# Optimization experiments

Measured on AMD Instinct MI355X. Metric: run time of the kernel, lower is better.

## Reference

```python
import jax, jax.numpy as jnp
import numpy as np

PARAMETER = 0.1
INPUT_SIZE = 512
OUTPUT_SIZE = 512


def setup_inputs() -> dict:
    key = jax.random.key(0)
    k1, k2, k3 = jax.random.split(key, 3)
    T, B = 4096, 32
    input_tensor = jax.random.normal(k1, (T, B, INPUT_SIZE), dtype=jnp.float32)
    k = np.sqrt(1.0 / INPUT_SIZE)
    weight = jax.random.uniform(k2, (OUTPUT_SIZE, INPUT_SIZE), dtype=jnp.float32, minval=-k, maxval=k)
    bias = jax.random.uniform(k3, (OUTPUT_SIZE,), dtype=jnp.float32, minval=-k, maxval=k)
    return {"input_tensor": input_tensor, "weight": weight, "bias": bias}


def reference(input_tensor, weight, bias):
    # linear projection: [T, B, I] @ [I, O] -> [T, B, O]
    y = jnp.einsum('tbi,oi->tbo', input_tensor, weight) + bias

    # EMA recurrence: v[0] = y[0]; v[t] = p * v[t-1] + y[t]
    def step(carry, yt):
        v = PARAMETER * carry + yt
        return v, v

    _, rest = jax.lax.scan(step, y[0], y[1:])
    return jnp.concatenate([y[:1], rest], axis=0)
```

## Files before the change

### kernel.cpp

```cpp
#include <hip/hip_runtime.h>
#include <hip/hip_bf16.h>

#define T_DIM 4096
#define B_DIM 32
#define I_DIM 512
#define O_DIM 512
#define M_DIM (T_DIM * B_DIM)
#define PARAM 0.1f
#define ISCALE 1.1111112f

#define STRIP 32
#define TAPS 8

#define BM 128
#define BN 128
#define BK 64
#define NK (I_DIM / BK)

typedef __attribute__((ext_vector_type(8))) short bf16x8;
typedef __attribute__((ext_vector_type(4))) float f32x4;

__device__ __forceinline__ unsigned short f2bf(float f) {
    union { __hip_bfloat16 b; unsigned short u; } cv;
    cv.b = __float2bfloat16(f);
    return cv.u;
}

__global__ __launch_bounds__(256) void wcvt_kernel(const float* __restrict__ W,
                                                   unsigned short* __restrict__ Wb) {
    const int i = (blockIdx.x * 256 + threadIdx.x) * 4;
    f32x4 v = *(const f32x4*)(W + i);
    ushort4 o;
    o.x = f2bf(v[0]); o.y = f2bf(v[1]); o.z = f2bf(v[2]); o.w = f2bf(v[3]);
    *(ushort4*)(Wb + i) = o;
}

__global__ __launch_bounds__(256) void xema_kernel(const float* __restrict__ X,
                                                   unsigned short* __restrict__ Xv) {
    const int s   = blockIdx.x >> 4;
    const int blk = blockIdx.x & 15;
    const int col = (blk * 256 + threadIdx.x) * 4;
    const int t0  = s * STRIP;
    const int b   = col >> 9;
    const int o   = col & 511;

    const float* xin = X + (size_t)t0 * 16384 + col;
    unsigned short* xout = Xv + (size_t)(t0 * 32 + b) * 512 + o;

    f32x4 v = {0.f, 0.f, 0.f, 0.f};
    if (s > 0) {
        const float* w = xin - (size_t)TAPS * 16384;
        #pragma unroll
        for (int j = 0; j < TAPS; ++j)
            v = PARAM * v + *(const f32x4*)(w + (size_t)j * 16384);
    }

    f32x4 bufA[4], bufB[4];
    #pragma unroll
    for (int j = 0; j < 4; ++j) bufA[j] = *(const f32x4*)(xin + (size_t)j * 16384);

    #pragma unroll
    for (int i = 0; i < STRIP; i += 8) {
        #pragma unroll
        for (int j = 0; j < 4; ++j)
            bufB[j] = *(const f32x4*)(xin + (size_t)(i + 4 + j) * 16384);
        #pragma unroll
        for (int j = 0; j < 4; ++j) {
            v = PARAM * v + bufA[j];
            ushort4 pk; pk.x = f2bf(v[0]); pk.y = f2bf(v[1]); pk.z = f2bf(v[2]); pk.w = f2bf(v[3]);
            *(ushort4*)(xout + (size_t)(i + j) * 16384) = pk;
        }
        if (i + 8 < STRIP) {
            #pragma unroll
            for (int j = 0; j < 4; ++j)
                bufA[j] = *(const f32x4*)(xin + (size_t)(i + 8 + j) * 16384);
        }
        #pragma unroll
        for (int j = 0; j < 4; ++j) {
            v = PARAM * v + bufB[j];
            ushort4 pk; pk.x = f2bf(v[0]); pk.y = f2bf(v[1]); pk.z = f2bf(v[2]); pk.w = f2bf(v[3]);
            *(ushort4*)(xout + (size_t)(i + 4 + j) * 16384) = pk;
        }
    }
}

__global__ __launch_bounds__(256, 4) void gemm_kernel(const unsigned short* __restrict__ Xv,
                                                      const unsigned short* __restrict__ Wb,
                                                      const float* __restrict__ bias,
                                                      float* __restrict__ Y) {
    __shared__ __align__(16) short As[BM * BK];
    __shared__ __align__(16) short Bs[BN * BK];

    const int tid  = threadIdx.x;
    const int lane = tid & 63;
    const int wave = tid >> 6;
    const int wm   = wave >> 1;
    const int wn   = wave & 1;

    const int bid = blockIdx.x;
    const int j   = bid >> 3;
    const int bn  = j & 3;
    const int mt  = (bid & 7) * 128 + (j >> 2);
    const int row0 = mt * BM;
    const int col0 = bn * BN;

    const int cs = (tid & 7) ^ ((tid >> 3) & 7);
    const unsigned short* aSrc = Xv + (size_t)(row0 + (tid >> 3)) * 512 + cs * 8;
    const unsigned short* bSrc = Wb + (size_t)(col0 + (tid >> 3)) * 512 + cs * 8;

    f32x4 acc[4][4] = {};

    for (int ks = 0; ks < NK; ++ks) {
        const int k0 = ks * BK;
        #pragma unroll
        for (int s_ = 0; s_ < 4; ++s_)
            __builtin_amdgcn_global_load_lds(
                (const __attribute__((address_space(1))) unsigned int*)(aSrc + (size_t)s_ * 32 * 512 + k0),
                (__attribute__((address_space(3))) unsigned int*)(As + (s_ * 256 + tid) * 8),
                16, 0, 0);
        #pragma unroll
        for (int s_ = 0; s_ < 4; ++s_)
            __builtin_amdgcn_global_load_lds(
                (const __attribute__((address_space(1))) unsigned int*)(bSrc + (size_t)s_ * 32 * 512 + k0),
                (__attribute__((address_space(3))) unsigned int*)(Bs + (s_ * 256 + tid) * 8),
                16, 0, 0);
        __syncthreads();

        #pragma unroll
        for (int kk = 0; kk < 2; ++kk) {
            const int cc = kk * 4 + (lane >> 4);
            bf16x8 a_[4], b_[4];
            #pragma unroll
            for (int mf = 0; mf < 4; ++mf) {
                const int r = wm * 64 + mf * 16 + (lane & 15);
                a_[mf] = *(const bf16x8*)((const char*)As + r * 128 + ((cc ^ (r & 7)) << 4));
            }
            #pragma unroll
            for (int nf = 0; nf < 4; ++nf) {
                const int r = wn * 64 + nf * 16 + (lane & 15);
                b_[nf] = *(const bf16x8*)((const char*)Bs + r * 128 + ((cc ^ (r & 7)) << 4));
            }
            #pragma unroll
            for (int mf = 0; mf < 4; ++mf)
                #pragma unroll
                for (int nf = 0; nf < 4; ++nf)
                    acc[mf][nf] = __builtin_amdgcn_mfma_f32_16x16x32_bf16(
                        a_[mf], b_[nf], acc[mf][nf], 0, 0, 0);
        }
        __syncthreads();
    }

    float sc[4][4];
    #pragma unroll
    for (int mf = 0; mf < 4; ++mf)
        #pragma unroll
        for (int jj = 0; jj < 4; ++jj) {
            const int t = (row0 + wm * 64 + mf * 16 + ((lane >> 4) << 2) + jj) >> 5;
            sc[mf][jj] = (1.0f - __expf(-2.3025851f * (float)(t + 1))) * ISCALE;
        }

    #pragma unroll
    for (int mf = 0; mf < 4; ++mf) {
        #pragma unroll
        for (int nf = 0; nf < 4; ++nf) {
            const int gcol = col0 + wn * 64 + nf * 16 + (lane & 15);
            const float bv = bias[gcol];
            #pragma unroll
            for (int jj = 0; jj < 4; ++jj) {
                const int grow = row0 + wm * 64 + mf * 16 + ((lane >> 4) << 2) + jj;
                Y[(size_t)grow * O_DIM + gcol] = acc[mf][nf][jj] + sc[mf][jj] * bv;
            }
        }
    }
}

extern "C" void kernel_launch(void* const* d_in, const int* in_sizes, int n_in,
                              void* d_out, int out_size, void* d_ws, size_t ws_size,
                              hipStream_t stream) {
    const float* X    = (const float*)d_in[0];
    const float* W    = (const float*)d_in[1];
    const float* bias = (const float*)d_in[2];
    float* Y = (float*)d_out;
    unsigned short* Wb = (unsigned short*)d_ws;
    unsigned short* Xv = (unsigned short*)((char*)d_ws + (1 << 20));

    wcvt_kernel<<<dim3(O_DIM * I_DIM / (256 * 4)), dim3(256), 0, stream>>>(W, Wb);
    xema_kernel<<<dim3((T_DIM / STRIP) * 16), dim3(256), 0, stream>>>(X, Xv);
    gemm_kernel<<<dim3((M_DIM / BM) * (O_DIM / BN)), dim3(256), 0, stream>>>(Xv, Wb, bias, Y);
}
```

Measured before the change: 236.5 us.

## Replace LDS-staged GEMM with direct global-to-register loads and wider tiles

The GEMM kernel drops LDS staging and barriers. Each wave now loads its bf16 A and B fragments straight from global memory into registers and computes a 128x64 tile, with the block covering 128x256. The grid halves, launch bounds drop to 2 blocks per CU, and the epilogue computes the bias scale per time step. This removes LDS traffic and synchronisation, but every wave re-reads the same A rows from global memory/cache and uses uncoalesced 16-byte row-strided loads, with more registers per thread.

Result: slower. 412.7 us (+74.5%).

```diff
diff --git a/kernel.cpp b/kernel.cpp
--- a/kernel.cpp
+++ b/kernel.cpp
@@ -11,11 +11,6 @@
 
 #define STRIP 32
 #define TAPS 8
-
-#define BM 128
-#define BN 128
-#define BK 64
-#define NK (I_DIM / BK)
 
 typedef __attribute__((ext_vector_type(8))) short bf16x8;
 typedef __attribute__((ext_vector_type(4))) float f32x4;
@@ -84,91 +79,73 @@
     }
 }
 
-__global__ __launch_bounds__(256, 4) void gemm_kernel(const unsigned short* __restrict__ Xv,
+__global__ __launch_bounds__(256, 2) void gemm_kernel(const unsigned short* __restrict__ Xv,
                                                       const unsigned short* __restrict__ Wb,
                                                       const float* __restrict__ bias,
                                                       float* __restrict__ Y) {
-    __shared__ __align__(16) short As[BM * BK];
-    __shared__ __align__(16) short Bs[BN * BK];
-
     const int tid  = threadIdx.x;
     const int lane = tid & 63;
     const int wave = tid >> 6;
-    const int wm   = wave >> 1;
-    const int wn   = wave & 1;
 
-    const int bid = blockIdx.x;
-    const int j   = bid >> 3;
-    const int bn  = j & 3;
-    const int mt  = (bid & 7) * 128 + (j >> 2);
-    const int row0 = mt * BM;
-    const int col0 = bn * BN;
+    const int bid  = blockIdx.x;
+    const int swz  = (bid & 7) * 256 + (bid >> 3);
+    const int bn   = swz & 1;
+    const int mg   = swz >> 1;
+    const int row0 = mg * 128;
+    const int col0 = bn * 256 + wave * 64;
 
-    const int cs = (tid & 7) ^ ((tid >> 3) & 7);
-    const unsigned short* aSrc = Xv + (size_t)(row0 + (tid >> 3)) * 512 + cs * 8;
-    const unsigned short* bSrc = Wb + (size_t)(col0 + (tid >> 3)) * 512 + cs * 8;
+    const unsigned short* aBase = Xv + (size_t)(row0 + (lane & 15)) * 512 + ((lane >> 4) << 3);
+    const unsigned short* bBase = Wb + (size_t)(col0 + (lane & 15)) * 512 + ((lane >> 4) << 3);
 
-    f32x4 acc[4][4] = {};
+    f32x4 acc[8][4] = {};
 
-    for (int ks = 0; ks < NK; ++ks) {
-        const int k0 = ks * BK;
+    #pragma unroll
+    for (int ks = 0; ks < 8; ++ks) {
+        bf16x8 a0[8], a1[8], b0[4], b1[4];
         #pragma unroll
-        for (int s_ = 0; s_ < 4; ++s_)
-            __builtin_amdgcn_global_load_lds(
-                (const __attribute__((address_space(1))) unsigned int*)(aSrc + (size_t)s_ * 32 * 512 + k0),
-                (__attribute__((address_space(3))) unsigned int*)(As + (s_ * 256 + tid) * 8),
-                16, 0, 0);
+        for (int nf = 0; nf < 4; ++nf) {
+            b0[nf] = *(const bf16x8*)(bBase + (size_t)nf * 16 * 512 + ks * 64);
+            b1[nf] = *(const bf16x8*)(bBase + (size_t)nf * 16 * 512 + ks * 64 + 32);
+        }
         #pragma unroll
-        for (int s_ = 0; s_ < 4; ++s_)
-            __builtin_amdgcn_global_load_lds(
-                (const __attribute__((address_space(1))) unsigned int*)(bSrc + (size_t)s_ * 32 * 512 + k0),
-                (__attribute__((address_space(3))) unsigned int*)(Bs + (s_ * 256 + tid) * 8),
-                16, 0, 0);
-        __syncthreads();
-
+        for (int mf = 0; mf < 8; ++mf) {
+            a0[mf] = *(const bf16x8*)(aBase + (size_t)mf * 16 * 512 + ks * 64);
+            a1[mf] = *(const bf16x8*)(aBase + (size_t)mf * 16 * 512 + ks * 64 + 32);
+        }
         #pragma unroll
-        for (int kk = 0; kk < 2; ++kk) {
-            const int cc = kk * 4 + (lane >> 4);
-            bf16x8 a_[4], b_[4];
+        for (int mf = 0; mf < 8; ++mf)
             #pragma unroll
-            for (int mf = 0; mf < 4; ++mf) {
-                const int r = wm * 64 + mf * 16 + (lane & 15);
-                a_[mf] = *(const bf16x8*)((const char*)As + r * 128 + ((cc ^ (r & 7)) << 4));
-            }
+            for (int nf = 0; nf < 4; ++nf)
+                acc[mf][nf] = __builtin_amdgcn_mfma_f32_16x16x32_bf16(
+                    a0[mf], b0[nf], acc[mf][nf], 0, 0, 0);
+        #pragma unroll
+        for (int mf = 0; mf < 8; ++mf)
             #pragma unroll
-            for (int nf = 0; nf < 4; ++nf) {
-                const int r = wn * 64 + nf * 16 + (lane & 15);
-                b_[nf] = *(const bf16x8*)((const char*)Bs + r * 128 + ((cc ^ (r & 7)) << 4));
-            }
-            #pragma unroll
-            for (int mf = 0; mf < 4; ++mf)
-                #pragma unroll
-                for (int nf = 0; nf < 4; ++nf)
-                    acc[mf][nf] = __builtin_amdgcn_mfma_f32_16x16x32_bf16(
-                        a_[mf], b_[nf], acc[mf][nf], 0, 0, 0);
-        }
-        __syncthreads();
+            for (int nf = 0; nf < 4; ++nf)
+                acc[mf][nf] = __builtin_amdgcn_mfma_f32_16x16x32_bf16(
+                    a1[mf], b1[nf], acc[mf][nf], 0, 0, 0);
     }
 
-    float sc[4][4];
+    float sc4[4];
     #pragma unroll
-    for (int mf = 0; mf < 4; ++mf)
-        #pragma unroll
-        for (int jj = 0; jj < 4; ++jj) {
-            const int t = (row0 + wm * 64 + mf * 16 + ((lane >> 4) << 2) + jj) >> 5;
-            sc[mf][jj] = (1.0f - __expf(-2.3025851f * (float)(t + 1))) * ISCALE;
-        }
+    for (int tt = 0; tt < 4; ++tt) {
+        const int t_ = (row0 >> 5) + tt;
+        sc4[tt] = (1.0f - __expf(-2.3025851f * (float)(t_ + 1))) * ISCALE;
+    }
+    float bv[4];
+    #pragma unroll
+    for (int nf = 0; nf < 4; ++nf)
+        bv[nf] = bias[col0 + nf * 16 + (lane & 15)];
 
     #pragma unroll
-    for (int mf = 0; mf < 4; ++mf) {
+    for (int mf = 0; mf < 8; ++mf) {
         #pragma unroll
         for (int nf = 0; nf < 4; ++nf) {
-            const int gcol = col0 + wn * 64 + nf * 16 + (lane & 15);
-            const float bv = bias[gcol];
+            const int gcol = col0 + nf * 16 + (lane & 15);
             #pragma unroll
-            for (int jj = 0; jj < 4; ++jj) {
-                const int grow = row0 + wm * 64 + mf * 16 + ((lane >> 4) << 2) + jj;
-                Y[(size_t)grow * O_DIM + gcol] = acc[mf][nf][jj] + sc[mf][jj] * bv;
+            for (int j = 0; j < 4; ++j) {
+                const int grow = row0 + mf * 16 + ((lane >> 4) << 2) + j;
+                Y[(size_t)grow * O_DIM + gcol] = acc[mf][nf][j] + sc4[mf >> 1] * bv[nf];
             }
         }
     }
@@ -186,5 +163,5 @@
 
     wcvt_kernel<<<dim3(O_DIM * I_DIM / (256 * 4)), dim3(256), 0, stream>>>(W, Wb);
     xema_kernel<<<dim3((T_DIM / STRIP) * 16), dim3(256), 0, stream>>>(X, Xv);
-    gemm_kernel<<<dim3((M_DIM / BM) * (O_DIM / BN)), dim3(256), 0, stream>>>(Xv, Wb, bias, Y);
+    gemm_kernel<<<dim3((M_DIM / 128) * 2), dim3(256), 0, stream>>>(Xv, Wb, bias, Y);
 }
```
